# Optimization experiments

Hardware: AMD Instinct MI355X
Metric: run time of the kernel (lower is better)

The kernel has to match this reference:

```python
import jax, jax.numpy as jnp
import numpy as np

D_MODEL = 1024
N_HEAD = 16
D_HEAD = 64
D_CAT = N_HEAD * D_HEAD
HD_MLP = 4096
LN_EPS = 1e-5


def setup_inputs() -> dict:
    key = jax.random.key(0)
    ks = jax.random.split(key, 12)
    bn, t = 2, 2048
    s = lambda fan_in: 1.0 / np.sqrt(fan_in)
    return {
        "x": jax.random.normal(ks[0], (bn, t, D_MODEL), dtype=jnp.float32),
        "mask": jnp.ones((bn, t), dtype=jnp.int32),
        "w_qkv": jax.random.normal(ks[1], (D_MODEL, 3 * D_CAT), dtype=jnp.float32) * s(D_MODEL),
        "w_tail": jax.random.normal(ks[2], (D_CAT, D_MODEL), dtype=jnp.float32) * s(D_CAT),
        "b_tail": jnp.zeros((D_MODEL,), dtype=jnp.float32),
        "ln1_g": jnp.ones((D_MODEL,), dtype=jnp.float32),
        "ln1_b": jnp.zeros((D_MODEL,), dtype=jnp.float32),
        "ln2_g": jnp.ones((D_MODEL,), dtype=jnp.float32),
        "ln2_b": jnp.zeros((D_MODEL,), dtype=jnp.float32),
        "w1": jax.random.normal(ks[3], (D_MODEL, HD_MLP), dtype=jnp.float32) * s(D_MODEL),
        "b1": jnp.zeros((HD_MLP,), dtype=jnp.float32),
        "w2": jax.random.normal(ks[4], (HD_MLP, D_MODEL), dtype=jnp.float32) * s(HD_MLP),
        "b2": jnp.zeros((D_MODEL,), dtype=jnp.float32),
    }


def _layer_norm(x, g, b):
    mu = jnp.mean(x, axis=-1, keepdims=True)
    var = jnp.mean(jnp.square(x - mu), axis=-1, keepdims=True)
    return (x - mu) * jax.lax.rsqrt(var + LN_EPS) * g + b


def _attention(z, mask, w_qkv, w_tail, b_tail):
    bn, t, _ = z.shape
    qkv = z @ w_qkv                      # (bn, t, 3*d_cat)
    qkv = qkv.reshape(bn, t, N_HEAD, 3, D_HEAD)  # chunk layout: per-head [q|k|v]
    q = qkv[..., 0, :].transpose(0, 2, 1, 3)     # (bn, h, t, dh)
    k = qkv[..., 1, :].transpose(0, 2, 1, 3)
    v = qkv[..., 2, :].transpose(0, 2, 1, 3)
    scale = D_HEAD ** -0.5
    dots = jnp.einsum("bhqd,bhkd->bhqk", q, k) * scale
    key_mask = (mask == 0)[:, None, None, :]     # (bn,1,1,t)
    dots = jnp.where(key_mask, -jnp.inf, dots)
    coef = jax.nn.softmax(dots, axis=-1)
    attn = jnp.einsum("bhqk,bhkd->bhqd", coef, v)
    out = attn.transpose(0, 2, 1, 3).reshape(bn, t, D_CAT)
    return out @ w_tail + b_tail


def reference(x, mask, w_qkv, w_tail, b_tail, ln1_g, ln1_b, ln2_g, ln2_b, w1, b1, w2, b2):
    z = _layer_norm(x, ln1_g, ln1_b)
    x = _attention(z, mask, w_qkv, w_tail, b_tail) + x
    z = _layer_norm(x, ln2_g, ln2_b)
    h = jax.nn.gelu(z @ w1 + b1, approximate=False)  # torch GELU default = exact erf
    x = h @ w2 + b2 + x
    return x
```

## Files before the change

### kernel.cpp

```cpp
#include <hip/hip_runtime.h>
#include <hip/hip_bf16.h>

#define DM 1024
#define TT 2048
#define NH 16
#define DH 64
#define HD 4096

typedef __attribute__((ext_vector_type(4))) float f32x4;
typedef __attribute__((ext_vector_type(8))) short s16x8;
typedef __attribute__((ext_vector_type(4))) short s16x4;

static __device__ __forceinline__ short f2bf(float f) {
  __hip_bfloat16 h = __float2bfloat16(f);
  return *reinterpret_cast<short*>(&h);
}

typedef const __attribute__((address_space(1))) char* gas1_t;
typedef __attribute__((address_space(3))) char* las3_t;
static __device__ __forceinline__ void glds16(const void* g, void* l) {
  __builtin_amdgcn_global_load_lds((gas1_t)g, (las3_t)l, 16, 0, 0);
}

__global__ __launch_bounds__(256) void transpose_cvt_k(
    const float* __restrict__ in, short* __restrict__ out, int K, int N)
{
  __shared__ float tile[32][33];
  const int n0 = blockIdx.x * 32, k0 = blockIdx.y * 32;
  const int tx = threadIdx.x & 31, ty = threadIdx.x >> 5;
#pragma unroll
  for (int i = 0; i < 4; ++i)
    tile[ty + i * 8][tx] = in[(size_t)(k0 + ty + i * 8) * N + n0 + tx];
  __syncthreads();
#pragma unroll
  for (int i = 0; i < 4; ++i) {
    int n = ty + i * 8;
    out[(size_t)(n0 + n) * K + k0 + tx] = f2bf(tile[tx][n]);
  }
}

__global__ __launch_bounds__(256) void ln_k(
    const float* __restrict__ x, const float* __restrict__ g,
    const float* __restrict__ b, short* __restrict__ out)
{
  const int row = blockIdx.x;
  const int tid = threadIdx.x;
  const float4 v = ((const float4*)(x + (size_t)row * DM))[tid];
  float s = v.x + v.y + v.z + v.w;
  float q = v.x * v.x + v.y * v.y + v.z * v.z + v.w * v.w;
#pragma unroll
  for (int off = 1; off < 64; off <<= 1) {
    s += __shfl_xor(s, off);
    q += __shfl_xor(q, off);
  }
  __shared__ float ss[4], sq[4];
  const int wave = tid >> 6;
  if ((tid & 63) == 0) { ss[wave] = s; sq[wave] = q; }
  __syncthreads();
  s = ss[0] + ss[1] + ss[2] + ss[3];
  q = sq[0] + sq[1] + sq[2] + sq[3];
  const float mu = s * (1.0f / DM);
  const float var = q * (1.0f / DM) - mu * mu;
  const float rs = rsqrtf(var + 1e-5f);
  const float4 gv = ((const float4*)g)[tid];
  const float4 bv = ((const float4*)b)[tid];
  s16x4 o;
  o[0] = f2bf((v.x - mu) * rs * gv.x + bv.x);
  o[1] = f2bf((v.y - mu) * rs * gv.y + bv.y);
  o[2] = f2bf((v.z - mu) * rs * gv.z + bv.z);
  o[3] = f2bf((v.w - mu) * rs * gv.w + bv.w);
  *(s16x4*)(out + (size_t)row * DM + tid * 4) = o;
}

template<int EPI>
__global__ __launch_bounds__(512, 4) void gemm_pipe(
    const short* __restrict__ A, const short* __restrict__ B,
    const float* __restrict__ bias, const float* __restrict__ res,
    float* __restrict__ outF, short* __restrict__ outB,
    short* __restrict__ outK, short* __restrict__ outV,
    int M, int N, int K)
{
  __shared__ short As[2][2][64 * 64];
  __shared__ short Bs[2][2][64 * 64];
  const int tid = threadIdx.x;
  const int wave = tid >> 6, lane = tid & 63;
  const int l15 = lane & 15, lhi = lane >> 4;
  const int bm = blockIdx.x, bn = blockIdx.y;
  const int wr = wave >> 2;
  const int wc = wave & 3;
  f32x4 acc[4][2] = {};

  const int srow = tid >> 2;
  const int scs = ((tid & 3) ^ ((srow >> 1) & 3)) * 16;
  const int ldst = srow * 64 + (tid & 3) * 16;
  const char* gA = (const char*)(A + (size_t)(bm * 128 + srow) * K);
  const char* gB = (const char*)(B + (size_t)(bn * 128 + srow) * K);

  const int NT = K >> 6;

  auto stagePair = [&](int buf, int kt, int kh) {
    const size_t go = (size_t)kt * 128 + kh * 64 + scs;
    glds16(gA + go, (char*)As[buf][kh] + ldst);
    glds16(gB + go, (char*)Bs[buf][kh] + ldst);
  };

  stagePair(0, 0, 0);
  stagePair(0, 0, 1);

  int buf = 0;
  for (int t = 0; t < NT; ++t) {
#pragma unroll
    for (int kh = 0; kh < 2; ++kh) {
      const bool more = (t + 1 < NT);
      if (more || kh == 0) asm volatile("s_waitcnt vmcnt(2)" ::: "memory");
      else                 asm volatile("s_waitcnt vmcnt(0)" ::: "memory");
      __builtin_amdgcn_s_barrier();
      __builtin_amdgcn_sched_barrier(0);
      s16x8 af[4], bfv[2];
#pragma unroll
      for (int m = 0; m < 4; ++m) {
        const int row = wr * 64 + m * 16 + l15;
        af[m] = *(const s16x8*)((const char*)As[buf][kh] + row * 64 +
                                ((lhi ^ ((row >> 1) & 3)) << 4));
      }
#pragma unroll
      for (int n = 0; n < 2; ++n) {
        const int row = wc * 32 + n * 16 + l15;
        bfv[n] = *(const s16x8*)((const char*)Bs[buf][kh] + row * 64 +
                                 ((lhi ^ ((row >> 1) & 3)) << 4));
      }
      if (more) stagePair(buf ^ 1, t + 1, kh);
      __builtin_amdgcn_s_setprio(1);
#pragma unroll
      for (int m = 0; m < 4; ++m)
#pragma unroll
        for (int n = 0; n < 2; ++n)
          acc[m][n] = __builtin_amdgcn_mfma_f32_16x16x32_bf16(af[m], bfv[n], acc[m][n], 0, 0, 0);
      __builtin_amdgcn_s_setprio(0);
    }
    buf ^= 1;
  }

  const int rowb = bm * 128 + wr * 64;
  const int colb = bn * 128 + wc * 32;
#pragma unroll
  for (int m = 0; m < 4; ++m) {
#pragma unroll
    for (int n = 0; n < 2; ++n) {
      if (EPI == 3) {
        const int col0 = colb + n * 16;
        const int h = col0 / 192;
        const int c0 = col0 - h * 192;
        const int region = c0 >> 6;
        const int d = (c0 & 63) + l15;
        const int row0 = rowb + m * 16 + lhi * 4;
        const int bb = row0 >> 11, tl0 = row0 & 2047;
        const size_t bh = (size_t)bb * NH + h;
        if (region == 2) {
          s16x4 pk;
#pragma unroll
          for (int rr = 0; rr < 4; ++rr) pk[rr] = f2bf(acc[m][n][rr]);
          *(s16x4*)(outV + (bh * 64 + d) * TT + tl0) = pk;
        } else {
          short* dst = (region == 0) ? outB : outK;
          const float qs = (region == 0) ? 0.18033688011112042f : 1.0f;
#pragma unroll
          for (int rr = 0; rr < 4; ++rr)
            dst[(bh * TT + tl0 + rr) * 64 + d] = f2bf(acc[m][n][rr] * qs);
        }
      } else {
        const int col = colb + n * 16 + l15;
        const float bv = bias[col];
#pragma unroll
        for (int rr = 0; rr < 4; ++rr) {
          const int row = rowb + m * 16 + lhi * 4 + rr;
          float v = acc[m][n][rr] + bv;
          if (EPI == 1) {
            v += res[(size_t)row * N + col];
            outF[(size_t)row * N + col] = v;
          } else {
            v = 0.5f * v * (1.0f + erff(v * 0.70710678118f));
            outB[(size_t)row * N + col] = f2bf(v);
          }
        }
      }
    }
  }
}

#define PSTRIDE 144
#define PFRAG   2304
__global__ __launch_bounds__(256, 4) void attn_k(
    const short* __restrict__ Qb, const short* __restrict__ Kb,
    const short* __restrict__ Vtb, const int* __restrict__ mask,
    short* __restrict__ outp)
{
  const int tid = threadIdx.x, wave = tid >> 6, lane = tid & 63;
  const int l15 = lane & 15, lhi = lane >> 4;
  const int lb = blockIdx.x;
  const int bh = lb & 31, qb = lb >> 5;
  const int b = bh >> 4, h = bh & 15;
  const int qw = qb * 64 + wave * 16;

  __shared__ short Ks[64 * 64];
  __shared__ short Vt[64 * 64];
  __shared__ char Ps[4 * PFRAG];

  const short* qp = Qb + ((size_t)bh * TT + qw + l15) * 64;
  const s16x8 aq0 = *(const s16x8*)(qp + lhi * 8);
  const s16x8 aq1 = *(const s16x8*)(qp + 32 + lhi * 8);

  f32x4 o[4] = {};
  float mrow = -1e30f, lrow = 0.f;

  const int kr_s = tid >> 2, kc_s = (tid & 3) * 16;
  const int ksw = (kr_s & 7) << 4;

  const short* kgb = Kb + (size_t)bh * TT * 64 + (size_t)kr_s * 64 + kc_s;
  const short* vgb = Vtb + ((size_t)bh * 64 + kr_s) * TT + kc_s;

  s16x8 kpre[2], vpre[2];
  kpre[0] = *(const s16x8*)kgb;       kpre[1] = *(const s16x8*)(kgb + 8);
  vpre[0] = *(const s16x8*)vgb;       vpre[1] = *(const s16x8*)(vgb + 8);
  int m0 = mask[b * TT + lane];

  char* pb = Ps + wave * PFRAG + l15 * PSTRIDE;

  for (int t0 = 0; t0 < TT; t0 += 64) {
    char* krow = (char*)Ks + kr_s * 128;
    *(s16x8*)(krow + ((kc_s * 2) ^ ksw)) = kpre[0];
    *(s16x8*)(krow + ((kc_s * 2 + 16) ^ ksw)) = kpre[1];
    char* vrow = (char*)Vt + kr_s * 128;
    *(s16x8*)(vrow + ((kc_s * 2) ^ ksw)) = vpre[0];
    *(s16x8*)(vrow + ((kc_s * 2 + 16) ^ ksw)) = vpre[1];
    __syncthreads();

    const unsigned long long mb0 = __ballot(m0 != 0);
    const bool full = mb0 == ~0ULL;

    if (t0 + 64 < TT) {
      const short* kg = kgb + (size_t)(t0 + 64) * 64;
      const short* vg = vgb + t0 + 64;
      kpre[0] = *(const s16x8*)kg;  kpre[1] = *(const s16x8*)(kg + 8);
      vpre[0] = *(const s16x8*)vg;  vpre[1] = *(const s16x8*)(vg + 8);
      m0 = mask[b * TT + t0 + 64 + lane];
    }

    f32x4 sv[4];
    __builtin_amdgcn_s_setprio(1);
#pragma unroll
    for (int n = 0; n < 4; ++n) {
      const int row = n * 16 + l15;
      const int sw = (row & 7) << 4;
      const char* kr = (const char*)Ks + row * 128;
      const s16x8 a0 = *(const s16x8*)(kr + ((lhi * 16) ^ sw));
      const s16x8 a1 = *(const s16x8*)(kr + ((64 + lhi * 16) ^ sw));
      f32x4 z = {};
      z = __builtin_amdgcn_mfma_f32_16x16x32_bf16(a0, aq0, z, 0, 0, 0);
      z = __builtin_amdgcn_mfma_f32_16x16x32_bf16(a1, aq1, z, 0, 0, 0);
      sv[n] = z;
    }
    __builtin_amdgcn_s_setprio(0);

    if (!full) {
#pragma unroll
      for (int n = 0; n < 4; ++n) {
        const unsigned nib = (unsigned)(mb0 >> (n * 16 + lhi * 4)) & 0xF;
#pragma unroll
        for (int rr = 0; rr < 4; ++rr)
          if (!((nib >> rr) & 1)) sv[n][rr] = -3e38f;
      }
    }

    float mx0 = fmaxf(sv[0][0], sv[1][0]), mx1 = fmaxf(sv[0][1], sv[1][1]);
    float mx2 = fmaxf(sv[0][2], sv[1][2]), mx3 = fmaxf(sv[0][3], sv[1][3]);
    mx0 = fmaxf(mx0, fmaxf(sv[2][0], sv[3][0]));
    mx1 = fmaxf(mx1, fmaxf(sv[2][1], sv[3][1]));
    mx2 = fmaxf(mx2, fmaxf(sv[2][2], sv[3][2]));
    mx3 = fmaxf(mx3, fmaxf(sv[2][3], sv[3][3]));
    float mx = fmaxf(fmaxf(mx0, mx1), fmaxf(mx2, mx3));
    mx = fmaxf(mx, __shfl_xor(mx, 16));
    mx = fmaxf(mx, __shfl_xor(mx, 32));
    if (__any(mx > mrow + 8.0f)) {
      const float mn = fmaxf(mrow, mx);
      const float alpha = exp2f(mrow - mn);
      mrow = mn;
      lrow *= alpha;
      float ar[4];
#pragma unroll
      for (int rr = 0; rr < 4; ++rr) ar[rr] = __shfl(alpha, lhi * 4 + rr);
#pragma unroll
      for (int db = 0; db < 4; ++db)
#pragma unroll
        for (int rr = 0; rr < 4; ++rr) o[db][rr] *= ar[rr];
    }
    float s0 = 0.f, s1 = 0.f, s2 = 0.f, s3 = 0.f;
#pragma unroll
    for (int n = 0; n < 4; ++n) {
      sv[n][0] = exp2f(sv[n][0] - mrow); s0 += sv[n][0];
      sv[n][1] = exp2f(sv[n][1] - mrow); s1 += sv[n][1];
      sv[n][2] = exp2f(sv[n][2] - mrow); s2 += sv[n][2];
      sv[n][3] = exp2f(sv[n][3] - mrow); s3 += sv[n][3];
    }
    float sum = (s0 + s1) + (s2 + s3);
    sum += __shfl_xor(sum, 16);
    sum += __shfl_xor(sum, 32);
    lrow += sum;

#pragma unroll
    for (int n = 0; n < 4; ++n) {
      s16x4 pk;
#pragma unroll
      for (int rr = 0; rr < 4; ++rr) pk[rr] = f2bf(sv[n][rr]);
      *(s16x4*)(pb + n * 32 + lhi * 8) = pk;
    }
    asm volatile("s_waitcnt lgkmcnt(0)" ::: "memory");
    __builtin_amdgcn_sched_barrier(0);
    s16x8 ap[2];
    ap[0] = *(const s16x8*)(pb + lhi * 16);
    ap[1] = *(const s16x8*)(pb + 64 + lhi * 16);

    __builtin_amdgcn_s_setprio(1);
#pragma unroll
    for (int db = 0; db < 4; ++db) {
      const int d = db * 16 + l15;
      const int swv = (d & 7) << 4;
      const char* vr2 = (const char*)Vt + d * 128;
#pragma unroll
      for (int ks = 0; ks < 2; ++ks) {
        const s16x8 bv = *(const s16x8*)(vr2 + ((ks * 64 + lhi * 16) ^ swv));
        o[db] = __builtin_amdgcn_mfma_f32_16x16x32_bf16(ap[ks], bv, o[db], 0, 0, 0);
      }
    }
    __builtin_amdgcn_s_setprio(0);
    __syncthreads();
  }

  float lr[4];
#pragma unroll
  for (int rr = 0; rr < 4; ++rr) lr[rr] = __shfl(lrow, lhi * 4 + rr);
#pragma unroll
  for (int db = 0; db < 4; ++db) {
#pragma unroll
    for (int rr = 0; rr < 4; ++rr) {
      const int qg = qw + lhi * 4 + rr;
      const int cg = h * 64 + db * 16 + l15;
      outp[(size_t)(b * TT + qg) * DM + cg] = f2bf(o[db][rr] / lr[rr]);
    }
  }
}

extern "C" void kernel_launch(void* const* d_in, const int* in_sizes, int n_in,
                              void* d_out, int out_size, void* d_ws, size_t ws_size,
                              hipStream_t stream)
{
  const float* x      = (const float*)d_in[0];
  const int*   mask   = (const int*)d_in[1];
  const float* w_qkv  = (const float*)d_in[2];
  const float* w_tail = (const float*)d_in[3];
  const float* b_tail = (const float*)d_in[4];
  const float* ln1g   = (const float*)d_in[5];
  const float* ln1b   = (const float*)d_in[6];
  const float* ln2g   = (const float*)d_in[7];
  const float* ln2b   = (const float*)d_in[8];
  const float* w1     = (const float*)d_in[9];
  const float* b1     = (const float*)d_in[10];
  const float* w2     = (const float*)d_in[11];
  const float* b2     = (const float*)d_in[12];

  char* ws = (char*)d_ws;
  size_t off = 0;
  auto take = [&](size_t bytes) {
    char* p = ws + off;
    off += (bytes + 255) & ~(size_t)255;
    return p;
  };
  short* slotW = (short*)take((size_t)4096 * 2048 * 2);
  short* slotZ = (short*)take((size_t)4096 * 1024 * 2);
  short* qb    = (short*)take((size_t)32 * 2048 * 64 * 2);
  short* kb    = (short*)take((size_t)32 * 2048 * 64 * 2);
  short* vtb   = (short*)take((size_t)32 * 64 * 2048 * 2);
  float* x1    = (float*)take((size_t)4096 * 1024 * 4);
  short* hbuf  = (short*)take((size_t)4096 * 4096 * 2);

  transpose_cvt_k<<<dim3(3072 / 32, 1024 / 32), 256, 0, stream>>>(w_qkv, slotW, 1024, 3072);
  ln_k<<<4096, 256, 0, stream>>>(x, ln1g, ln1b, slotZ);
  gemm_pipe<3><<<dim3(32, 24), 512, 0, stream>>>(slotZ, slotW, nullptr, nullptr,
                                                 nullptr, qb, kb, vtb, 4096, 3072, 1024);
  attn_k<<<1024, 256, 0, stream>>>(qb, kb, vtb, mask, slotZ);
  transpose_cvt_k<<<dim3(1024 / 32, 1024 / 32), 256, 0, stream>>>(w_tail, slotW, 1024, 1024);
  gemm_pipe<1><<<dim3(32, 8), 512, 0, stream>>>(slotZ, slotW, b_tail, x,
                                                x1, nullptr, nullptr, nullptr, 4096, 1024, 1024);
  ln_k<<<4096, 256, 0, stream>>>(x1, ln2g, ln2b, slotZ);
  transpose_cvt_k<<<dim3(4096 / 32, 1024 / 32), 256, 0, stream>>>(w1, slotW, 1024, 4096);
  gemm_pipe<2><<<dim3(32, 32), 512, 0, stream>>>(slotZ, slotW, b1, nullptr,
                                                 nullptr, hbuf, nullptr, nullptr, 4096, 4096, 1024);
  transpose_cvt_k<<<dim3(1024 / 32, 4096 / 32), 256, 0, stream>>>(w2, slotW, 4096, 1024);
  gemm_pipe<1><<<dim3(32, 8), 512, 0, stream>>>(hbuf, slotW, b2, x1,
                                                (float*)d_out, nullptr, nullptr, nullptr, 4096, 1024, 4096);
}
```

Before: 265.9 us.

## Add wider 128x256-tile GEMM kernel for the MLP up-projection

Adds a new gemm_pipe_w kernel that computes a 128x256 output tile per 512-thread block, with 8 waves arranged 2x4 and each wave holding a 64x64 accumulator. It double-buffers 64-wide K slices through LDS using direct global-to-LDS loads with an XOR swizzle. The W1 GEMM with GELU epilogue switches to this kernel, halving the grid along N. The aim is more operand reuse per LDS load, at the cost of more registers per thread and fewer blocks in flight.

```diff
diff --git a/kernel.cpp b/kernel.cpp
--- a/kernel.cpp
+++ b/kernel.cpp
@@ -188,6 +188,100 @@
   }
 }
 
+template<int EPI>
+__global__ __launch_bounds__(512, 2) void gemm_pipe_w(
+    const short* __restrict__ A, const short* __restrict__ B,
+    const float* __restrict__ bias, const float* __restrict__ res,
+    float* __restrict__ outF, short* __restrict__ outB,
+    int M, int N, int K)
+{
+  __shared__ short As[2][2][64 * 64];
+  __shared__ short Bs[2][2][128 * 64];
+  const int tid = threadIdx.x;
+  const int wave = tid >> 6, lane = tid & 63;
+  const int l15 = lane & 15, lhi = lane >> 4;
+  const int bm = blockIdx.x, bn = blockIdx.y;
+  const int wr = wave >> 2;
+  const int wc = wave & 3;
+  f32x4 acc[4][4] = {};
+
+  const int srow = tid >> 2;
+  const int scs = ((tid & 3) ^ ((srow >> 1) & 3)) * 16;
+  const int ldst = srow * 64 + (tid & 3) * 16;
+  const char* gA  = (const char*)(A + (size_t)(bm * 128 + srow) * K);
+  const char* gB0 = (const char*)(B + (size_t)(bn * 256 + srow) * K);
+  const char* gB1 = gB0 + (size_t)128 * K * 2;
+
+  const int NT = K >> 6;
+
+  auto stageTrip = [&](int buf, int kt, int kh) {
+    const size_t go = (size_t)kt * 128 + kh * 64 + scs;
+    glds16(gA + go,  (char*)As[buf][kh] + ldst);
+    glds16(gB0 + go, (char*)Bs[buf][kh] + ldst);
+    glds16(gB1 + go, (char*)Bs[buf][kh] + 8192 + ldst);
+  };
+
+  stageTrip(0, 0, 0);
+  stageTrip(0, 0, 1);
+
+  int buf = 0;
+  for (int t = 0; t < NT; ++t) {
+#pragma unroll
+    for (int kh = 0; kh < 2; ++kh) {
+      const bool more = (t + 1 < NT);
+      if (more || kh == 0) asm volatile("s_waitcnt vmcnt(3)" ::: "memory");
+      else                 asm volatile("s_waitcnt vmcnt(0)" ::: "memory");
+      __builtin_amdgcn_s_barrier();
+      __builtin_amdgcn_sched_barrier(0);
+      s16x8 af[4], bfv[4];
+#pragma unroll
+      for (int m = 0; m < 4; ++m) {
+        const int row = wr * 64 + m * 16 + l15;
+        af[m] = *(const s16x8*)((const char*)As[buf][kh] + row * 64 +
+                                ((lhi ^ ((row >> 1) & 3)) << 4));
+      }
+#pragma unroll
+      for (int n = 0; n < 4; ++n) {
+        const int row = wc * 64 + n * 16 + l15;
+        bfv[n] = *(const s16x8*)((const char*)Bs[buf][kh] + row * 64 +
+                                 ((lhi ^ ((row >> 1) & 3)) << 4));
+      }
+      if (more) stageTrip(buf ^ 1, t + 1, kh);
+      __builtin_amdgcn_s_setprio(1);
+#pragma unroll
+      for (int m = 0; m < 4; ++m)
+#pragma unroll
+        for (int n = 0; n < 4; ++n)
+          acc[m][n] = __builtin_amdgcn_mfma_f32_16x16x32_bf16(af[m], bfv[n], acc[m][n], 0, 0, 0);
+      __builtin_amdgcn_s_setprio(0);
+    }
+    buf ^= 1;
+  }
+
+  const int rowb = bm * 128 + wr * 64;
+  const int colb = bn * 256 + wc * 64;
+#pragma unroll
+  for (int m = 0; m < 4; ++m) {
+#pragma unroll
+    for (int n = 0; n < 4; ++n) {
+      const int col = colb + n * 16 + l15;
+      const float bv = bias[col];
+#pragma unroll
+      for (int rr = 0; rr < 4; ++rr) {
+        const int row = rowb + m * 16 + lhi * 4 + rr;
+        float v = acc[m][n][rr] + bv;
+        if (EPI == 1) {
+          v += res[(size_t)row * N + col];
+          outF[(size_t)row * N + col] = v;
+        } else {
+          v = 0.5f * v * (1.0f + erff(v * 0.70710678118f));
+          outB[(size_t)row * N + col] = f2bf(v);
+        }
+      }
+    }
+  }
+}
+
 #define PSTRIDE 144
 #define PFRAG   2304
 __global__ __launch_bounds__(256, 4) void attn_k(
@@ -393,8 +487,8 @@
                                                 x1, nullptr, nullptr, nullptr, 4096, 1024, 1024);
   ln_k<<<4096, 256, 0, stream>>>(x1, ln2g, ln2b, slotZ);
   transpose_cvt_k<<<dim3(4096 / 32, 1024 / 32), 256, 0, stream>>>(w1, slotW, 1024, 4096);
-  gemm_pipe<2><<<dim3(32, 32), 512, 0, stream>>>(slotZ, slotW, b1, nullptr,
-                                                 nullptr, hbuf, nullptr, nullptr, 4096, 4096, 1024);
+  gemm_pipe_w<2><<<dim3(32, 16), 512, 0, stream>>>(slotZ, slotW, b1, nullptr,
+                                                   nullptr, hbuf, 4096, 4096, 1024);
   transpose_cvt_k<<<dim3(1024 / 32, 4096 / 32), 256, 0, stream>>>(w2, slotW, 4096, 1024);
   gemm_pipe<1><<<dim3(32, 8), 512, 0, stream>>>(hbuf, slotW, b2, x1,
                                                 (float*)d_out, nullptr, nullptr, nullptr, 4096, 1024, 4096);
```

Result: no change. 267.1 us (+0.5%).

## Double-buffer attention K/V via direct-to-LDS loads and merge weight transposes

Applied to the files above, without the earlier changes.

The attention kernel now double-buffers K and V tiles in shared memory. It fills them with global_load_lds asynchronous copies issued one tile ahead, with a swizzled source address, and waits on them with vmcnt instead of staging through registers. Occupancy bounds drop from 4 to 3 blocks per CU to make room for the larger LDS footprint. Separately, the four weight transpose/convert launches are merged into one kernel that writes separate buffers, which removes three launches and lets those transposes run together.

```diff
diff --git a/kernel.cpp b/kernel.cpp
--- a/kernel.cpp
+++ b/kernel.cpp
@@ -22,11 +22,20 @@
   __builtin_amdgcn_global_load_lds((gas1_t)g, (las3_t)l, 16, 0, 0);
 }
 
-__global__ __launch_bounds__(256) void transpose_cvt_k(
-    const float* __restrict__ in, short* __restrict__ out, int K, int N)
+__global__ __launch_bounds__(256) void transpose_all_k(
+    const float* __restrict__ wqkv, const float* __restrict__ wtail,
+    const float* __restrict__ w1,   const float* __restrict__ w2,
+    short* __restrict__ oqkv, short* __restrict__ otail,
+    short* __restrict__ o1,   short* __restrict__ o2)
 {
   __shared__ float tile[32][33];
-  const int n0 = blockIdx.x * 32, k0 = blockIdx.y * 32;
+  int t = blockIdx.x;
+  const float* in; short* out; int K, N, nx;
+  if (t < 3072)      {          in = wqkv;  out = oqkv;  K = 1024; N = 3072; nx = 96; }
+  else if (t < 4096) { t -= 3072; in = wtail; out = otail; K = 1024; N = 1024; nx = 32; }
+  else if (t < 8192) { t -= 4096; in = w1;    out = o1;    K = 1024; N = 4096; nx = 128; }
+  else               { t -= 8192; in = w2;    out = o2;    K = 4096; N = 1024; nx = 32; }
+  const int n0 = (t % nx) * 32, k0 = (t / nx) * 32;
   const int tx = threadIdx.x & 31, ty = threadIdx.x >> 5;
 #pragma unroll
   for (int i = 0; i < 4; ++i)
@@ -190,7 +199,7 @@
 
 #define PSTRIDE 144
 #define PFRAG   2304
-__global__ __launch_bounds__(256, 4) void attn_k(
+__global__ __launch_bounds__(256, 3) void attn_k(
     const short* __restrict__ Qb, const short* __restrict__ Kb,
     const short* __restrict__ Vtb, const int* __restrict__ mask,
     short* __restrict__ outp)
@@ -202,8 +211,8 @@
   const int b = bh >> 4, h = bh & 15;
   const int qw = qb * 64 + wave * 16;
 
-  __shared__ short Ks[64 * 64];
-  __shared__ short Vt[64 * 64];
+  __shared__ short Ks[2][64 * 64];
+  __shared__ short Vt[2][64 * 64];
   __shared__ char Ps[4 * PFRAG];
 
   const short* qp = Qb + ((size_t)bh * TT + qw + l15) * 64;
@@ -213,38 +222,39 @@
   f32x4 o[4] = {};
   float mrow = -1e30f, lrow = 0.f;
 
-  const int kr_s = tid >> 2, kc_s = (tid & 3) * 16;
-  const int ksw = (kr_s & 7) << 4;
-
-  const short* kgb = Kb + (size_t)bh * TT * 64 + (size_t)kr_s * 64 + kc_s;
-  const short* vgb = Vtb + ((size_t)bh * 64 + kr_s) * TT + kc_s;
-
-  s16x8 kpre[2], vpre[2];
-  kpre[0] = *(const s16x8*)kgb;       kpre[1] = *(const s16x8*)(kgb + 8);
-  vpre[0] = *(const s16x8*)vgb;       vpre[1] = *(const s16x8*)(vgb + 8);
-  int m0 = mask[b * TT + lane];
-
-  char* pb = Ps + wave * PFRAG + l15 * PSTRIDE;
-
-  for (int t0 = 0; t0 < TT; t0 += 64) {
-    char* krow = (char*)Ks + kr_s * 128;
-    *(s16x8*)(krow + ((kc_s * 2) ^ ksw)) = kpre[0];
-    *(s16x8*)(krow + ((kc_s * 2 + 16) ^ ksw)) = kpre[1];
-    char* vrow = (char*)Vt + kr_s * 128;
-    *(s16x8*)(vrow + ((kc_s * 2) ^ ksw)) = vpre[0];
-    *(s16x8*)(vrow + ((kc_s * 2 + 16) ^ ksw)) = vpre[1];
-    __syncthreads();
-
-    const unsigned long long mb0 = __ballot(m0 != 0);
+  const int c7 = tid & 7, r5 = tid >> 3;
+  const int sch = (c7 ^ (r5 & 7)) * 16;
+  const char* srcK = (const char*)(Kb + (size_t)bh * TT * 64) + r5 * 128 + sch;
+  const char* srcV = (const char*)(Vtb + (size_t)bh * 64 * TT) + (size_t)r5 * 4096 + sch;
+  const int ldstB = tid * 16;
+
+  glds16(srcK, (char*)Ks[0] + ldstB);
+  glds16(srcK + 4096, (char*)Ks[0] + ldstB + 4096);
+  glds16(srcV, (char*)Vt[0] + ldstB);
+  glds16(srcV + 32 * 4096, (char*)Vt[0] + ldstB + 4096);
+  int mcur = mask[b * TT + lane];
+
+  const int NT = TT / 64;
+  int buf = 0;
+  for (int t = 0; t < NT; ++t) {
+    int mnext = 0;
+    if (t + 1 < NT) {
+      mnext = mask[b * TT + (t + 1) * 64 + lane];
+      const char* sk = srcK + (size_t)(t + 1) * 8192;
+      const char* sv = srcV + (size_t)(t + 1) * 128;
+      char* dk = (char*)Ks[buf ^ 1] + ldstB;
+      char* dv = (char*)Vt[buf ^ 1] + ldstB;
+      glds16(sk, dk);             glds16(sk + 4096, dk + 4096);
+      glds16(sv, dv);             glds16(sv + 32 * 4096, dv + 4096);
+      asm volatile("s_waitcnt vmcnt(5)" ::: "memory");
+    } else {
+      asm volatile("s_waitcnt vmcnt(0)" ::: "memory");
+    }
+    __builtin_amdgcn_s_barrier();
+    __builtin_amdgcn_sched_barrier(0);
+
+    const unsigned long long mb0 = __ballot(mcur != 0);
     const bool full = mb0 == ~0ULL;
-
-    if (t0 + 64 < TT) {
-      const short* kg = kgb + (size_t)(t0 + 64) * 64;
-      const short* vg = vgb + t0 + 64;
-      kpre[0] = *(const s16x8*)kg;  kpre[1] = *(const s16x8*)(kg + 8);
-      vpre[0] = *(const s16x8*)vg;  vpre[1] = *(const s16x8*)(vg + 8);
-      m0 = mask[b * TT + t0 + 64 + lane];
-    }
 
     f32x4 sv[4];
     __builtin_amdgcn_s_setprio(1);
@@ -252,7 +262,7 @@
     for (int n = 0; n < 4; ++n) {
       const int row = n * 16 + l15;
       const int sw = (row & 7) << 4;
-      const char* kr = (const char*)Ks + row * 128;
+      const char* kr = (const char*)Ks[buf] + row * 128;
       const s16x8 a0 = *(const s16x8*)(kr + ((lhi * 16) ^ sw));
       const s16x8 a1 = *(const s16x8*)(kr + ((64 + lhi * 16) ^ sw));
       f32x4 z = {};
@@ -307,6 +317,7 @@
     sum += __shfl_xor(sum, 32);
     lrow += sum;
 
+    char* pb = Ps + wave * PFRAG + l15 * PSTRIDE;
 #pragma unroll
     for (int n = 0; n < 4; ++n) {
       s16x4 pk;
@@ -325,7 +336,7 @@
     for (int db = 0; db < 4; ++db) {
       const int d = db * 16 + l15;
       const int swv = (d & 7) << 4;
-      const char* vr2 = (const char*)Vt + d * 128;
+      const char* vr2 = (const char*)Vt[buf] + d * 128;
 #pragma unroll
       for (int ks = 0; ks < 2; ++ks) {
         const s16x8 bv = *(const s16x8*)(vr2 + ((ks * 64 + lhi * 16) ^ swv));
@@ -333,7 +344,9 @@
       }
     }
     __builtin_amdgcn_s_setprio(0);
-    __syncthreads();
+    __builtin_amdgcn_s_barrier();
+    mcur = mnext;
+    buf ^= 1;
   }
 
   float lr[4];
@@ -375,7 +388,10 @@
     off += (bytes + 255) & ~(size_t)255;
     return p;
   };
-  short* slotW = (short*)take((size_t)4096 * 2048 * 2);
+  short* wqkvT = (short*)take((size_t)3072 * 1024 * 2);
+  short* wtailT= (short*)take((size_t)1024 * 1024 * 2);
+  short* w1T   = (short*)take((size_t)4096 * 1024 * 2);
+  short* w2T   = (short*)take((size_t)1024 * 4096 * 2);
   short* slotZ = (short*)take((size_t)4096 * 1024 * 2);
   short* qb    = (short*)take((size_t)32 * 2048 * 64 * 2);
   short* kb    = (short*)take((size_t)32 * 2048 * 64 * 2);
@@ -383,19 +399,17 @@
   float* x1    = (float*)take((size_t)4096 * 1024 * 4);
   short* hbuf  = (short*)take((size_t)4096 * 4096 * 2);
 
-  transpose_cvt_k<<<dim3(3072 / 32, 1024 / 32), 256, 0, stream>>>(w_qkv, slotW, 1024, 3072);
+  transpose_all_k<<<12288, 256, 0, stream>>>(w_qkv, w_tail, w1, w2,
+                                             wqkvT, wtailT, w1T, w2T);
   ln_k<<<4096, 256, 0, stream>>>(x, ln1g, ln1b, slotZ);
-  gemm_pipe<3><<<dim3(32, 24), 512, 0, stream>>>(slotZ, slotW, nullptr, nullptr,
+  gemm_pipe<3><<<dim3(32, 24), 512, 0, stream>>>(slotZ, wqkvT, nullptr, nullptr,
                                                  nullptr, qb, kb, vtb, 4096, 3072, 1024);
   attn_k<<<1024, 256, 0, stream>>>(qb, kb, vtb, mask, slotZ);
-  transpose_cvt_k<<<dim3(1024 / 32, 1024 / 32), 256, 0, stream>>>(w_tail, slotW, 1024, 1024);
-  gemm_pipe<1><<<dim3(32, 8), 512, 0, stream>>>(slotZ, slotW, b_tail, x,
+  gemm_pipe<1><<<dim3(32, 8), 512, 0, stream>>>(slotZ, wtailT, b_tail, x,
                                                 x1, nullptr, nullptr, nullptr, 4096, 1024, 1024);
   ln_k<<<4096, 256, 0, stream>>>(x1, ln2g, ln2b, slotZ);
-  transpose_cvt_k<<<dim3(4096 / 32, 1024 / 32), 256, 0, stream>>>(w1, slotW, 1024, 4096);
-  gemm_pipe<2><<<dim3(32, 32), 512, 0, stream>>>(slotZ, slotW, b1, nullptr,
+  gemm_pipe<2><<<dim3(32, 32), 512, 0, stream>>>(slotZ, w1T, b1, nullptr,
                                                  nullptr, hbuf, nullptr, nullptr, 4096, 4096, 1024);
-  transpose_cvt_k<<<dim3(1024 / 32, 4096 / 32), 256, 0, stream>>>(w2, slotW, 4096, 1024);
-  gemm_pipe<1><<<dim3(32, 8), 512, 0, stream>>>(hbuf, slotW, b2, x1,
+  gemm_pipe<1><<<dim3(32, 8), 512, 0, stream>>>(hbuf, w2T, b2, x1,
                                                 (float*)d_out, nullptr, nullptr, nullptr, 4096, 1024, 4096);
 }
```

Result: slower. 274.3 us (+3.2%).
